# Kernel optimization log

Hardware: AMD Instinct MI355X
Metric: run time of the kernel (lower is better)

Reference implementation:

```python
import jax, jax.numpy as jnp
import numpy as np

B = 1 << 21          # shading points per batch
U_RES, CH = 400, 8   # spatial plane
A_RES, ACH = 50, 50 and 8  # placeholder, real consts below
A_RES, ACH = 50, 8   # angular planes (h/d)
HID = 32
IN_CH = CH + 2 * ACH  # 24


def _bilerp_clamp(tex, uv):
    # Bilinear interp, both axes clamped (U-plane). tex: (H,W,C), uv: (B,2) in [0,1]
    H, W, _ = tex.shape
    u = jnp.clip(uv[:, 0], 0.0, 1.0) * (W - 1)
    v = jnp.clip(uv[:, 1], 0.0, 1.0) * (H - 1)
    x0 = jnp.floor(u).astype(jnp.int32)
    x1 = jnp.clip(x0 + 1, 0, W - 1)
    y0 = jnp.floor(v).astype(jnp.int32)
    y1 = jnp.clip(y0 + 1, 0, H - 1)
    ur = (u - x0.astype(u.dtype))[:, None]
    vr = (v - y0.astype(v.dtype))[:, None]
    p00 = tex[y0, x0]; p10 = tex[y0, x1]; p01 = tex[y1, x0]; p11 = tex[y1, x1]
    return ((1 - ur) * (1 - vr) * p00 + ur * (1 - vr) * p10
            + (1 - ur) * vr * p01 + ur * vr * p11)


def _bilerp_wrap_u(tex, uv):
    # Bilinear interp wrapping the u (phi) axis, clamping v (H/D planes).
    H, W, _ = tex.shape
    u = (uv[:, 0] % 1.0) * W
    v = jnp.clip(uv[:, 1], 0.0, 1.0) * (H - 1)
    x0f = jnp.floor(u)
    x0 = x0f.astype(jnp.int32) % W
    x1 = (x0 + 1) % W
    y0 = jnp.floor(v).astype(jnp.int32)
    y1 = jnp.clip(y0 + 1, 0, H - 1)
    ur = (u - x0f)[:, None]
    vr = (v - y0.astype(v.dtype))[:, None]
    p00 = tex[y0, x0]; p10 = tex[y0, x1]; p01 = tex[y1, x0]; p11 = tex[y1, x1]
    return ((1 - ur) * (1 - vr) * p00 + ur * (1 - vr) * p10
            + (1 - ur) * vr * p01 + ur * vr * p11)


def setup_inputs() -> dict:
    key = jax.random.key(0)
    ks = jax.random.split(key, 8)
    x = jax.random.uniform(ks[0], (B, 6), dtype=jnp.float32)
    u_plane = 0.01 * jax.random.normal(ks[1], (U_RES, U_RES, CH), dtype=jnp.float32)
    h_plane = 0.01 * jax.random.normal(ks[2], (A_RES, A_RES, ACH), dtype=jnp.float32)
    d_plane = 0.01 * jax.random.normal(ks[3], (A_RES, A_RES, ACH), dtype=jnp.float32)
    def lin_w(k, fout, fin):  # torch nn.Linear default init (kaiming-uniform-ish)
        lim = 1.0 / np.sqrt(fin)
        return jax.random.uniform(k, (fout, fin), jnp.float32, -lim, lim)
    W0 = lin_w(ks[4], HID, IN_CH)
    W1 = lin_w(ks[5], HID, HID)
    W2 = lin_w(ks[6], HID, HID)
    W3 = lin_w(ks[7], 3, HID)
    return {"x": x, "u_plane": u_plane, "h_plane": h_plane, "d_plane": d_plane,
            "W0": W0, "W1": W1, "W2": W2, "W3": W3}


def reference(x, u_plane, h_plane, d_plane, W0, W1, W2, W3):
    # Split and reorder: H/D planes receive (u=phi, v=theta)
    uv = x[:, 0:2]
    h_uv = jnp.stack((x[:, 3], x[:, 2]), axis=1)
    d_uv = jnp.stack((x[:, 5], x[:, 4]), axis=1)
    fU = _bilerp_clamp(u_plane, uv)       # (B, CH)
    fH = _bilerp_wrap_u(h_plane, h_uv)    # (B, ACH)
    fD = _bilerp_wrap_u(d_plane, d_uv)    # (B, ACH)
    feat = jnp.concatenate([fU, fH, fD], axis=1)  # (B, 24)
    # Quant mode 'off' -> QLinear is a plain bias-free matmul with W^T
    h = jax.nn.relu(feat @ W0.T)
    h = jax.nn.relu(h @ W1.T)
    h = jax.nn.relu(h @ W2.T)
    return h @ W3.T  # (B, 3)
```

## Files before the change

kernel.cpp:

```cpp
#include <hip/hip_runtime.h>

typedef _Float16 half4 __attribute__((ext_vector_type(4)));
typedef _Float16 half8 __attribute__((ext_vector_type(8)));
typedef float floatx4 __attribute__((ext_vector_type(4)));

#define U_RESV 400
#define A_RESV 50

#define UHALVES (U_RESV * U_RESV * 8)
#define AHALVES (A_RESV * A_RESV * 8)
#define WOFF    (UHALVES + 2 * AHALVES)
#define W0OFF   0
#define W1OFF   896
#define W2OFF   2048
#define W3OFF   3200
#define WTOT    3776

__device__ __forceinline__ float clamp01(float x) { return fminf(fmaxf(x, 0.0f), 1.0f); }

__device__ __forceinline__ floatx4 mfma16(half4 a, half4 b, floatx4 c) {
    return __builtin_amdgcn_mfma_f32_16x16x16f16(a, b, c, 0, 0, 0);
}
__device__ __forceinline__ half4 zero4() {
    half4 h; h[0] = h[1] = h[2] = h[3] = (_Float16)0.f; return h;
}
__device__ __forceinline__ half4 relu4(half4 v) {
#if __has_builtin(__builtin_elementwise_max)
    return __builtin_elementwise_max(v, zero4());
#else
    half4 r;
#pragma unroll
    for (int i = 0; i < 4; ++i) r[i] = v[i] > (_Float16)0.f ? v[i] : (_Float16)0.f;
    return r;
#endif
}

__device__ __forceinline__ void cvt_chunk(const float* __restrict__ src,
                                          _Float16* __restrict__ dst, int i) {
    float4 a = *(const float4*)(src + (size_t)i * 8);
    float4 b = *(const float4*)(src + (size_t)i * 8 + 4);
    half8 h;
    h[0] = (_Float16)a.x; h[1] = (_Float16)a.y; h[2] = (_Float16)a.z; h[3] = (_Float16)a.w;
    h[4] = (_Float16)b.x; h[5] = (_Float16)b.y; h[6] = (_Float16)b.z; h[7] = (_Float16)b.w;
    *(half8*)(dst + (size_t)i * 8) = h;
}

__device__ __forceinline__ void wblob_fill(const float* __restrict__ W0,
                                           const float* __restrict__ W1,
                                           const float* __restrict__ W2,
                                           const float* __restrict__ W3,
                                           _Float16* __restrict__ w, int tid, int nthr) {
    for (int i = tid; i < WTOT; i += nthr) {
        float v;
        if (i < W1OFF) {
            int r = i / 28, c = i - r * 28;
            v = (c < 24) ? W0[r * 24 + c] : 0.f;
        } else if (i < W2OFF) {
            int j = i - W1OFF, r = j / 36, c = j - r * 36;
            v = (c < 32) ? W1[r * 32 + c] : 0.f;
        } else if (i < W3OFF) {
            int j = i - W2OFF, r = j / 36, c = j - r * 36;
            v = (c < 32) ? W2[r * 32 + c] : 0.f;
        } else {
            int j = i - W3OFF, r = j / 36, c = j - r * 36;
            v = (r < 3 && c < 32) ? W3[r * 32 + c] : 0.f;
        }
        w[i] = (_Float16)v;
    }
}

__global__ __launch_bounds__(256) void pconv_kernel(
    const float* __restrict__ u_plane, const float* __restrict__ h_plane,
    const float* __restrict__ d_plane, const float* __restrict__ W0,
    const float* __restrict__ W1, const float* __restrict__ W2,
    const float* __restrict__ W3, _Float16* __restrict__ dst) {
    const int gid = blockIdx.x * 256 + threadIdx.x;
    const int gsz = gridDim.x * 256;
    for (int i = gid; i < UHALVES / 8; i += gsz) cvt_chunk(u_plane, dst, i);
    for (int i = gid; i < AHALVES / 8; i += gsz) cvt_chunk(h_plane, dst + UHALVES, i);
    for (int i = gid; i < AHALVES / 8; i += gsz) cvt_chunk(d_plane, dst + UHALVES + AHALVES, i);
    if (blockIdx.x == 0) wblob_fill(W0, W1, W2, W3, dst + WOFF, threadIdx.x, 256);
}

__global__ __launch_bounds__(256) void wprep_kernel(
    const float* __restrict__ W0, const float* __restrict__ W1,
    const float* __restrict__ W2, const float* __restrict__ W3,
    _Float16* __restrict__ wdst) {
    wblob_fill(W0, W1, W2, W3, wdst, threadIdx.x, 256);
}

struct GA { int o0, o1, o2, o3; float w00, w10, w01, w11; };

__device__ __forceinline__ GA mkU(float ux, float uy) {
    GA g;
    float u = clamp01(ux) * (float)(U_RESV - 1);
    float v = clamp01(uy) * (float)(U_RESV - 1);
    float x0f = floorf(u), y0f = floorf(v);
    int x0 = (int)x0f, y0 = (int)y0f;
    int x1 = min(x0 + 1, U_RESV - 1), y1 = min(y0 + 1, U_RESV - 1);
    float ur = u - x0f, vr = v - y0f;
    g.w00 = (1.0f - ur) * (1.0f - vr); g.w10 = ur * (1.0f - vr);
    g.w01 = (1.0f - ur) * vr;          g.w11 = ur * vr;
    g.o0 = (y0 * U_RESV + x0) * 8;
    g.o1 = (y0 * U_RESV + x1) * 8;
    g.o2 = (y1 * U_RESV + x0) * 8;
    g.o3 = (y1 * U_RESV + x1) * 8;
    return g;
}
__device__ __forceinline__ GA mkA(float uu, float vv) {
    GA g;
    float uf = uu - floorf(uu);
    float u = uf * (float)A_RESV;
    float v = clamp01(vv) * (float)(A_RESV - 1);
    float x0f = floorf(u), y0f = floorf(v);
    int x0 = (int)x0f;
    int x1 = x0 + 1; if (x1 == A_RESV) x1 = 0;
    int y0 = (int)y0f;
    int y1 = min(y0 + 1, A_RESV - 1);
    float ur = u - x0f, vr = v - y0f;
    g.w00 = (1.0f - ur) * (1.0f - vr); g.w10 = ur * (1.0f - vr);
    g.w01 = (1.0f - ur) * vr;          g.w11 = ur * vr;
    g.o0 = (y0 * A_RESV + x0) * 8;
    g.o1 = (y0 * A_RESV + x1) * 8;
    g.o2 = (y1 * A_RESV + x0) * 8;
    g.o3 = (y1 * A_RESV + x1) * 8;
    return g;
}

__device__ __forceinline__ void blend8(half8 a, half8 b, half8 c, half8 d,
                                       const GA& g, float* f) {
#pragma unroll
    for (int i = 0; i < 8; ++i) {
        float r = (float)a[i] * g.w00;
        r = fmaf((float)b[i], g.w10, r);
        r = fmaf((float)c[i], g.w01, r);
        r = fmaf((float)d[i], g.w11, r);
        f[i] = r;
    }
}


template <int K>
__global__ __launch_bounds__(1024, 4) void tpmlp_kernel(
    const float* __restrict__ x,
    const _Float16* __restrict__ up,
    const _Float16* __restrict__ hdsrc,
    const _Float16* __restrict__ wsw,
    float* __restrict__ out) {
    const int tid  = threadIdx.x;
    const int lane = tid & 63;
    const int wv   = tid >> 6;
    const int q    = lane >> 4;
    const int c15  = lane & 15;

    __shared__ __align__(16) _Float16 fl[1024 * 28];
    __shared__ __align__(16) _Float16 hdl[2 * AHALVES];
    __shared__ __align__(16) _Float16 wl[WTOT];

    {
        const uint4* src = (const uint4*)hdsrc;
        uint4* dst = (uint4*)hdl;
        for (int i = tid; i < (2 * AHALVES) / 8; i += 1024) dst[i] = src[i];
        if (tid < 472) ((uint4*)wl)[tid] = ((const uint4*)wsw)[tid];
    }
    __syncthreads();

    const _Float16* hp  = hdl;
    const _Float16* dp  = hdl + AHALVES;
    const _Float16* wb  = fl + (size_t)wv * 64 * 28;
    const _Float16* w0l = wl + W0OFF;
    const _Float16* w1l = wl + W1OFF;
    const _Float16* w2l = wl + W2OFF;
    const _Float16* w3l = wl + W3OFF;
    const size_t blkbase = (size_t)blockIdx.x * (1024 * K);

#pragma unroll 1
    for (int it = 0; it < K; ++it) {
        const size_t P = blkbase + (size_t)it * 1024 + tid;

        const float2* xp = (const float2*)(x + P * 6);
        float2 p01v = xp[0], p23v = xp[1], p45v = xp[2];

        GA gU = mkU(p01v.x, p01v.y);
        GA gH = mkA(p23v.y, p23v.x);
        GA gD = mkA(p45v.y, p45v.x);

        half8 tU0 = *(const half8*)(up + gU.o0);
        half8 tU1 = *(const half8*)(up + gU.o1);
        half8 tU2 = *(const half8*)(up + gU.o2);
        half8 tU3 = *(const half8*)(up + gU.o3);
        __builtin_amdgcn_sched_barrier(0);

        half8 tH0 = *(const half8*)(hp + gH.o0);
        half8 tH1 = *(const half8*)(hp + gH.o1);
        half8 tH2 = *(const half8*)(hp + gH.o2);
        half8 tH3 = *(const half8*)(hp + gH.o3);
        half8 tD0 = *(const half8*)(dp + gD.o0);
        half8 tD1 = *(const half8*)(dp + gD.o1);
        half8 tD2 = *(const half8*)(dp + gD.o2);
        half8 tD3 = *(const half8*)(dp + gD.o3);

        float fU[8], fH[8], fD[8];
        blend8(tH0, tH1, tH2, tH3, gH, fH);
        blend8(tD0, tD1, tD2, tD3, gD, fD);
        blend8(tU0, tU1, tU2, tU3, gU, fU);

        {
            _Float16* row = fl + tid * 28;
            half8 hU, hH, hD;
#pragma unroll
            for (int i = 0; i < 8; ++i) {
                hU[i] = (_Float16)fU[i];
                hH[i] = (_Float16)fH[i];
                hD[i] = (_Float16)fD[i];
            }
            *(half8*)(row)      = hU;
            *(half8*)(row + 8)  = hH;
            *(half8*)(row + 16) = hD;
        }
        asm volatile("s_waitcnt lgkmcnt(0)" ::: "memory");
        __builtin_amdgcn_sched_barrier(0);

        floatx4 zf; zf[0] = 0.f; zf[1] = 0.f; zf[2] = 0.f; zf[3] = 0.f;
        half4 b0[4], b1[4];
#pragma unroll
        for (int j = 0; j < 4; ++j) {
            const _Float16* r = wb + (size_t)(j * 16 + c15) * 28;
            b0[j] = *(const half4*)(r + q * 4);
            b1[j] = (q < 2) ? *(const half4*)(r + 16 + q * 4) : zero4();
        }

        floatx4 cc[2][4];
#pragma unroll
        for (int m = 0; m < 2; ++m) {
            half4 a0 = *(const half4*)(w0l + (size_t)(16 * m + c15) * 28 + q * 4);
            half4 a1 = (q < 2) ? *(const half4*)(w0l + (size_t)(16 * m + c15) * 28 + 16 + q * 4) : zero4();
#pragma unroll
            for (int j = 0; j < 4; ++j)
                cc[m][j] = mfma16(a1, b1[j], mfma16(a0, b0[j], zf));
        }
#pragma unroll
        for (int j = 0; j < 4; ++j) {
#pragma unroll
            for (int e = 0; e < 4; ++e) {
                b0[j][e] = (_Float16)cc[0][j][e];
                b1[j][e] = (_Float16)cc[1][j][e];
            }
            b0[j] = relu4(b0[j]);
            b1[j] = relu4(b1[j]);
        }

#pragma unroll
        for (int m = 0; m < 2; ++m) {
            half4 a0 = *(const half4*)(w1l + (size_t)(16 * m + c15) * 36 + q * 4);
            half4 a1 = *(const half4*)(w1l + (size_t)(16 * m + c15) * 36 + 16 + q * 4);
#pragma unroll
            for (int j = 0; j < 4; ++j)
                cc[m][j] = mfma16(a1, b1[j], mfma16(a0, b0[j], zf));
        }
#pragma unroll
        for (int j = 0; j < 4; ++j) {
#pragma unroll
            for (int e = 0; e < 4; ++e) {
                b0[j][e] = (_Float16)cc[0][j][e];
                b1[j][e] = (_Float16)cc[1][j][e];
            }
            b0[j] = relu4(b0[j]);
            b1[j] = relu4(b1[j]);
        }

#pragma unroll
        for (int m = 0; m < 2; ++m) {
            half4 a0 = *(const half4*)(w2l + (size_t)(16 * m + c15) * 36 + q * 4);
            half4 a1 = *(const half4*)(w2l + (size_t)(16 * m + c15) * 36 + 16 + q * 4);
#pragma unroll
            for (int j = 0; j < 4; ++j)
                cc[m][j] = mfma16(a1, b1[j], mfma16(a0, b0[j], zf));
        }
#pragma unroll
        for (int j = 0; j < 4; ++j) {
#pragma unroll
            for (int e = 0; e < 4; ++e) {
                b0[j][e] = (_Float16)cc[0][j][e];
                b1[j][e] = (_Float16)cc[1][j][e];
            }
            b0[j] = relu4(b0[j]);
            b1[j] = relu4(b1[j]);
        }

        floatx4 c3[4];
        {
            half4 a0 = *(const half4*)(w3l + (size_t)c15 * 36 + q * 4);
            half4 a1 = *(const half4*)(w3l + (size_t)c15 * 36 + 16 + q * 4);
#pragma unroll
            for (int j = 0; j < 4; ++j)
                c3[j] = mfma16(a1, b1[j], mfma16(a0, b0[j], zf));
        }

        if (lane < 16) {
            const size_t base = blkbase + (size_t)it * 1024 + (size_t)wv * 64;
#pragma unroll
            for (int j = 0; j < 4; ++j) {
                size_t p = base + (size_t)j * 16 + lane;
                float* o = out + p * 3;
                o[0] = c3[j][0];
                o[1] = c3[j][1];
                o[2] = c3[j][2];
            }
        }
    }
}

__global__ __launch_bounds__(512, 2) void tpmlp_f32(
    const float* __restrict__ x,
    const float* __restrict__ up,
    const float* __restrict__ hp,
    const float* __restrict__ dp,
    const _Float16* __restrict__ wsw,
    float* __restrict__ out) {
    const int tid  = threadIdx.x;
    const int lane = tid & 63;
    const int wv   = tid >> 6;
    const int q    = lane >> 4;
    const int c15  = lane & 15;

    __shared__ __align__(16) _Float16 fl[512 * 28];
    __shared__ __align__(16) _Float16 wl[WTOT];

    const size_t P = (size_t)blockIdx.x * 512 + tid;
    const float2* xp = (const float2*)(x + P * 6);
    float2 p01v = xp[0], p23v = xp[1], p45v = xp[2];

    uint4 w_a;
    if (tid < 472) w_a = ((const uint4*)wsw)[tid];

    GA gU = mkU(p01v.x, p01v.y);
    GA gH = mkA(p23v.y, p23v.x);
    GA gD = mkA(p45v.y, p45v.x);

    float4 sU0 = *(const float4*)(up + gU.o0); float4 rU0 = *(const float4*)(up + gU.o0 + 4);
    float4 sU1 = *(const float4*)(up + gU.o1); float4 rU1 = *(const float4*)(up + gU.o1 + 4);
    float4 sU2 = *(const float4*)(up + gU.o2); float4 rU2 = *(const float4*)(up + gU.o2 + 4);
    float4 sU3 = *(const float4*)(up + gU.o3); float4 rU3 = *(const float4*)(up + gU.o3 + 4);
    float4 sH0 = *(const float4*)(hp + gH.o0); float4 rH0 = *(const float4*)(hp + gH.o0 + 4);
    float4 sH1 = *(const float4*)(hp + gH.o1); float4 rH1 = *(const float4*)(hp + gH.o1 + 4);
    float4 sH2 = *(const float4*)(hp + gH.o2); float4 rH2 = *(const float4*)(hp + gH.o2 + 4);
    float4 sH3 = *(const float4*)(hp + gH.o3); float4 rH3 = *(const float4*)(hp + gH.o3 + 4);
    float4 sD0 = *(const float4*)(dp + gD.o0); float4 rD0 = *(const float4*)(dp + gD.o0 + 4);
    float4 sD1 = *(const float4*)(dp + gD.o1); float4 rD1 = *(const float4*)(dp + gD.o1 + 4);
    float4 sD2 = *(const float4*)(dp + gD.o2); float4 rD2 = *(const float4*)(dp + gD.o2 + 4);
    float4 sD3 = *(const float4*)(dp + gD.o3); float4 rD3 = *(const float4*)(dp + gD.o3 + 4);
    __builtin_amdgcn_sched_barrier(0);

    if (tid < 472) ((uint4*)wl)[tid] = w_a;
    asm volatile("s_waitcnt lgkmcnt(0)" ::: "memory");
    __builtin_amdgcn_s_barrier();

    float fU[8], fH[8], fD[8];
#pragma unroll
    for (int i = 0; i < 8; ++i) {
        const float* a = i < 4 ? (const float*)&sU0 : (const float*)&rU0;
        const float* b = i < 4 ? (const float*)&sU1 : (const float*)&rU1;
        const float* c = i < 4 ? (const float*)&sU2 : (const float*)&rU2;
        const float* d = i < 4 ? (const float*)&sU3 : (const float*)&rU3;
        int k = i & 3;
        float r = a[k] * gU.w00;
        r = fmaf(b[k], gU.w10, r);
        r = fmaf(c[k], gU.w01, r);
        r = fmaf(d[k], gU.w11, r);
        fU[i] = r;
    }
#pragma unroll
    for (int i = 0; i < 8; ++i) {
        const float* a = i < 4 ? (const float*)&sH0 : (const float*)&rH0;
        const float* b = i < 4 ? (const float*)&sH1 : (const float*)&rH1;
        const float* c = i < 4 ? (const float*)&sH2 : (const float*)&rH2;
        const float* d = i < 4 ? (const float*)&sH3 : (const float*)&rH3;
        int k = i & 3;
        float r = a[k] * gH.w00;
        r = fmaf(b[k], gH.w10, r);
        r = fmaf(c[k], gH.w01, r);
        r = fmaf(d[k], gH.w11, r);
        fH[i] = r;
    }
#pragma unroll
    for (int i = 0; i < 8; ++i) {
        const float* a = i < 4 ? (const float*)&sD0 : (const float*)&rD0;
        const float* b = i < 4 ? (const float*)&sD1 : (const float*)&rD1;
        const float* c = i < 4 ? (const float*)&sD2 : (const float*)&rD2;
        const float* d = i < 4 ? (const float*)&sD3 : (const float*)&rD3;
        int k = i & 3;
        float r = a[k] * gD.w00;
        r = fmaf(b[k], gD.w10, r);
        r = fmaf(c[k], gD.w01, r);
        r = fmaf(d[k], gD.w11, r);
        fD[i] = r;
    }

    {
        _Float16* row = fl + tid * 28;
        half8 hU, hH, hD;
#pragma unroll
        for (int i = 0; i < 8; ++i) {
            hU[i] = (_Float16)fU[i];
            hH[i] = (_Float16)fH[i];
            hD[i] = (_Float16)fD[i];
        }
        *(half8*)(row)      = hU;
        *(half8*)(row + 8)  = hH;
        *(half8*)(row + 16) = hD;
    }
    asm volatile("s_waitcnt lgkmcnt(0)" ::: "memory");
    __builtin_amdgcn_sched_barrier(0);

    floatx4 zf; zf[0] = 0.f; zf[1] = 0.f; zf[2] = 0.f; zf[3] = 0.f;
    const _Float16* wb = fl + (size_t)wv * 64 * 28;
    const _Float16* w0l = wl + W0OFF;
    const _Float16* w1l = wl + W1OFF;
    const _Float16* w2l = wl + W2OFF;
    const _Float16* w3l = wl + W3OFF;

    half4 b0[4], b1[4];
#pragma unroll
    for (int j = 0; j < 4; ++j) {
        const _Float16* r = wb + (size_t)(j * 16 + c15) * 28;
        b0[j] = *(const half4*)(r + q * 4);
        b1[j] = (q < 2) ? *(const half4*)(r + 16 + q * 4) : zero4();
    }

    floatx4 cc[2][4];
#pragma unroll
    for (int m = 0; m < 2; ++m) {
        half4 a0 = *(const half4*)(w0l + (size_t)(16 * m + c15) * 28 + q * 4);
        half4 a1 = (q < 2) ? *(const half4*)(w0l + (size_t)(16 * m + c15) * 28 + 16 + q * 4) : zero4();
#pragma unroll
        for (int j = 0; j < 4; ++j)
            cc[m][j] = mfma16(a1, b1[j], mfma16(a0, b0[j], zf));
    }
#pragma unroll
    for (int j = 0; j < 4; ++j) {
#pragma unroll
        for (int e = 0; e < 4; ++e) {
            b0[j][e] = (_Float16)cc[0][j][e];
            b1[j][e] = (_Float16)cc[1][j][e];
        }
        b0[j] = relu4(b0[j]);
        b1[j] = relu4(b1[j]);
    }
#pragma unroll
    for (int m = 0; m < 2; ++m) {
        half4 a0 = *(const half4*)(w1l + (size_t)(16 * m + c15) * 36 + q * 4);
        half4 a1 = *(const half4*)(w1l + (size_t)(16 * m + c15) * 36 + 16 + q * 4);
#pragma unroll
        for (int j = 0; j < 4; ++j)
            cc[m][j] = mfma16(a1, b1[j], mfma16(a0, b0[j], zf));
    }
#pragma unroll
    for (int j = 0; j < 4; ++j) {
#pragma unroll
        for (int e = 0; e < 4; ++e) {
            b0[j][e] = (_Float16)cc[0][j][e];
            b1[j][e] = (_Float16)cc[1][j][e];
        }
        b0[j] = relu4(b0[j]);
        b1[j] = relu4(b1[j]);
    }
#pragma unroll
    for (int m = 0; m < 2; ++m) {
        half4 a0 = *(const half4*)(w2l + (size_t)(16 * m + c15) * 36 + q * 4);
        half4 a1 = *(const half4*)(w2l + (size_t)(16 * m + c15) * 36 + 16 + q * 4);
#pragma unroll
        for (int j = 0; j < 4; ++j)
            cc[m][j] = mfma16(a1, b1[j], mfma16(a0, b0[j], zf));
    }
#pragma unroll
    for (int j = 0; j < 4; ++j) {
#pragma unroll
        for (int e = 0; e < 4; ++e) {
            b0[j][e] = (_Float16)cc[0][j][e];
            b1[j][e] = (_Float16)cc[1][j][e];
        }
        b0[j] = relu4(b0[j]);
        b1[j] = relu4(b1[j]);
    }

    floatx4 c3[4];
    {
        half4 a0 = *(const half4*)(w3l + (size_t)c15 * 36 + q * 4);
        half4 a1 = *(const half4*)(w3l + (size_t)c15 * 36 + 16 + q * 4);
#pragma unroll
        for (int j = 0; j < 4; ++j)
            c3[j] = mfma16(a1, b1[j], mfma16(a0, b0[j], zf));
    }

    if (lane < 16) {
        const size_t base = (size_t)blockIdx.x * 512 + (size_t)wv * 64;
#pragma unroll
        for (int j = 0; j < 4; ++j) {
            size_t p = base + (size_t)j * 16 + lane;
            float* o = out + p * 3;
            o[0] = c3[j][0];
            o[1] = c3[j][1];
            o[2] = c3[j][2];
        }
    }
}

extern "C" void kernel_launch(void* const* d_in, const int* in_sizes, int n_in,
                              void* d_out, int out_size, void* d_ws, size_t ws_size,
                              hipStream_t stream) {
    const float* x       = (const float*)d_in[0];
    const float* u_plane = (const float*)d_in[1];
    const float* h_plane = (const float*)d_in[2];
    const float* d_plane = (const float*)d_in[3];
    const float* W0      = (const float*)d_in[4];
    const float* W1      = (const float*)d_in[5];
    const float* W2      = (const float*)d_in[6];
    const float* W3      = (const float*)d_in[7];
    float* out = (float*)d_out;
    _Float16* wsw = (_Float16*)d_ws;

    int n = in_sizes[0] / 6;
    constexpr int K = 2;

    const size_t need = ((size_t)WOFF + WTOT) * 2;
    if (ws_size >= need) {
        pconv_kernel<<<648, 256, 0, stream>>>(u_plane, h_plane, d_plane,
                                              W0, W1, W2, W3, wsw);
        int grid = n / (1024 * K);
        tpmlp_kernel<K><<<grid, 1024, 0, stream>>>(
            x, wsw, wsw + UHALVES, wsw + WOFF, out);
    } else {
        wprep_kernel<<<1, 256, 0, stream>>>(W0, W1, W2, W3, wsw);
        tpmlp_f32<<<n / 512, 512, 0, stream>>>(
            x, u_plane, h_plane, d_plane, wsw, out);
    }
}
```

Measured before the change: 67.01 us.

## Software-pipeline x loads and U-plane gathers across iterations, raise K to 4

Prefetches the next iteration's x coordinates and U-plane texel gathers from global memory while the current iteration does its H/D blends and MLP, with x loaded two iterations ahead. The loop is fully unrolled, and each block now handles 4 chunks of 1024 points instead of 2. The aim is to hide global gather latency behind compute. In exchange, register pressure rises from the extra live half8 values, and the grid is halved, which may reduce occupancy and parallelism across CUs.

```diff
diff --git a/kernel.cpp b/kernel.cpp
--- a/kernel.cpp
+++ b/kernel.cpp
@@ -174,23 +174,40 @@
     const _Float16* w3l = wl + W3OFF;
     const size_t blkbase = (size_t)blockIdx.x * (1024 * K);
 
-#pragma unroll 1
+    auto xload = [&](int it, float2& a, float2& b, float2& c) {
+        const float2* p = (const float2*)(x + (blkbase + (size_t)it * 1024 + tid) * 6);
+        a = p[0]; b = p[1]; c = p[2];
+    };
+
+    float2 xc01, xc23, xc45;
+    float2 xn01, xn23, xn45;
+    xload(0, xc01, xc23, xc45);
+    if (K > 1) xload(1, xn01, xn23, xn45);
+
+    GA gUc = mkU(xc01.x, xc01.y);
+    half8 tU0 = *(const half8*)(up + gUc.o0);
+    half8 tU1 = *(const half8*)(up + gUc.o1);
+    half8 tU2 = *(const half8*)(up + gUc.o2);
+    half8 tU3 = *(const half8*)(up + gUc.o3);
+    __builtin_amdgcn_sched_barrier(0);
+
+#pragma unroll
     for (int it = 0; it < K; ++it) {
-        const size_t P = blkbase + (size_t)it * 1024 + tid;
-
-        const float2* xp = (const float2*)(x + P * 6);
-        float2 p01v = xp[0], p23v = xp[1], p45v = xp[2];
-
-        GA gU = mkU(p01v.x, p01v.y);
-        GA gH = mkA(p23v.y, p23v.x);
-        GA gD = mkA(p45v.y, p45v.x);
-
-        half8 tU0 = *(const half8*)(up + gU.o0);
-        half8 tU1 = *(const half8*)(up + gU.o1);
-        half8 tU2 = *(const half8*)(up + gU.o2);
-        half8 tU3 = *(const half8*)(up + gU.o3);
+        GA gUn;
+        half8 mU0, mU1, mU2, mU3;
+        float2 x201, x223, x245;
+        if (it + 1 < K) {
+            gUn = mkU(xn01.x, xn01.y);
+            mU0 = *(const half8*)(up + gUn.o0);
+            mU1 = *(const half8*)(up + gUn.o1);
+            mU2 = *(const half8*)(up + gUn.o2);
+            mU3 = *(const half8*)(up + gUn.o3);
+        }
+        if (it + 2 < K) xload(it + 2, x201, x223, x245);
         __builtin_amdgcn_sched_barrier(0);
 
+        GA gH = mkA(xc23.y, xc23.x);
+        GA gD = mkA(xc45.y, xc45.x);
         half8 tH0 = *(const half8*)(hp + gH.o0);
         half8 tH1 = *(const half8*)(hp + gH.o1);
         half8 tH2 = *(const half8*)(hp + gH.o2);
@@ -203,7 +220,7 @@
         float fU[8], fH[8], fD[8];
         blend8(tH0, tH1, tH2, tH3, gH, fH);
         blend8(tD0, tD1, tD2, tD3, gD, fD);
-        blend8(tU0, tU1, tU2, tU3, gU, fU);
+        blend8(tU0, tU1, tU2, tU3, gUc, fU);
 
         {
             _Float16* row = fl + tid * 28;
@@ -307,6 +324,13 @@
                 o[1] = c3[j][1];
                 o[2] = c3[j][2];
             }
+        }
+
+        if (it + 1 < K) {
+            xc01 = xn01; xc23 = xn23; xc45 = xn45;
+            xn01 = x201; xn23 = x223; xn45 = x245;
+            gUc = gUn;
+            tU0 = mU0; tU1 = mU1; tU2 = mU2; tU3 = mU3;
         }
     }
 }
@@ -521,7 +545,7 @@
     _Float16* wsw = (_Float16*)d_ws;
 
     int n = in_sizes[0] / 6;
-    constexpr int K = 2;
+    constexpr int K = 4;
 
     const size_t need = ((size_t)WOFF + WTOT) * 2;
     if (ws_size >= need) {
```

Measured after the change: 65.02 us. 1.03x faster.
